# Kernel tuning notes

Measured on AMD Instinct MI355X. Metric: run time of the kernel, lower is better.

Reference implementation:

```python
import jax, jax.numpy as jnp
import numpy as np

N_ITERATIONS = 3
EPS = 1e-07


def squash(t, axis=-1):
    sqr_norm = jnp.sum(t * t, axis=axis, keepdims=True)
    norm = jnp.sqrt(sqr_norm + EPS)
    return sqr_norm * t / ((1.0 + sqr_norm) * norm)


def setup_inputs() -> dict:
    key = jax.random.key(0)
    B, N_IN, N_OUT, D = 256, 1152, 10, 16
    u_hat = jax.random.normal(key, (B, N_IN, N_OUT, D, 1), dtype=jnp.float32)
    return {"u_hat": u_hat}


def reference(u_hat):
    # u_hat: [B, n_in, n_out, d, 1]
    B, n_in, n_out = u_hat.shape[0], u_hat.shape[1], u_hat.shape[2]
    b = jnp.zeros((B, n_in, n_out, 1, 1), dtype=u_hat.dtype)
    v = None
    for r in range(N_ITERATIONS):
        c = jax.nn.softmax(b, axis=1)                      # softmax over input caps
        s = jnp.sum(c * u_hat, axis=1, keepdims=True)      # [B, 1, n_out, d, 1]
        v = squash(s, axis=-2)                             # squash over capsule dim
        if r < N_ITERATIONS - 1:
            # u_hat^T @ v (broadcast v over input caps): agreement [B, n_in, n_out, 1, 1]
            a = jnp.sum(u_hat * v, axis=-2, keepdims=True)
            b = b + a
    return jnp.squeeze(v, axis=1)                          # [B, n_out, d, 1]
```

## Files before the change

kernel.cpp:

```cpp
#include <hip/hip_runtime.h>

#define BATCH 256
#define NIN   1152
#define NOUT  10
#define DDIM  16
#define KPT   18

__global__ __launch_bounds__(256)
void routing_kernel(const float* __restrict__ u_hat, float* __restrict__ out) {
    __shared__ float bsh[NIN];
    __shared__ float wsh[NIN];
    __shared__ float red[4 * DDIM];
    __shared__ float vsh[DDIM];
    __shared__ float scal[8];

    const int t    = threadIdx.x;
    const int q    = t & 3;
    const int g    = t >> 2;
    const int wave = t >> 6;
    const int lane = t & 63;

    const int bb = blockIdx.x / NOUT;
    const int oo = blockIdx.x % NOUT;

    const float* base = u_hat + (size_t)bb * (NIN * NOUT * DDIM) + oo * DDIM + q * 4;

    float4 u[KPT];
#pragma unroll
    for (int k = 0; k < KPT; ++k) {
        const int i = g + 64 * k;
        u[k] = *reinterpret_cast<const float4*>(base + (size_t)i * (NOUT * DDIM));
    }

    for (int i = t; i < NIN; i += 256) bsh[i] = 0.0f;
    __syncthreads();

    for (int r = 0; r < 3; ++r) {
        float m = -3.4e38f;
        for (int i = t; i < NIN; i += 256) m = fmaxf(m, bsh[i]);
        for (int off = 32; off >= 1; off >>= 1) m = fmaxf(m, __shfl_down(m, off));
        if (lane == 0) scal[wave] = m;
        __syncthreads();
        m = fmaxf(fmaxf(scal[0], scal[1]), fmaxf(scal[2], scal[3]));

        float z = 0.0f;
        for (int i = t; i < NIN; i += 256) {
            const float w = __expf(bsh[i] - m);
            wsh[i] = w;
            z += w;
        }
        for (int off = 32; off >= 1; off >>= 1) z += __shfl_down(z, off);
        if (lane == 0) scal[4 + wave] = z;
        __syncthreads();
        const float invZ = 1.0f / (scal[4] + scal[5] + scal[6] + scal[7]);

        float sx = 0.f, sy = 0.f, sz = 0.f, sw = 0.f;
#pragma unroll
        for (int k = 0; k < KPT; ++k) {
            const float w = wsh[g + 64 * k];
            sx += w * u[k].x; sy += w * u[k].y; sz += w * u[k].z; sw += w * u[k].w;
        }
        for (int off = 32; off >= 4; off >>= 1) {
            sx += __shfl_down(sx, off);
            sy += __shfl_down(sy, off);
            sz += __shfl_down(sz, off);
            sw += __shfl_down(sw, off);
        }
        if (lane < 4) {
            float* rp = &red[wave * DDIM + lane * 4];
            rp[0] = sx; rp[1] = sy; rp[2] = sz; rp[3] = sw;
        }
        __syncthreads();
        if (t < DDIM) {
            vsh[t] = (red[t] + red[DDIM + t] + red[2 * DDIM + t] + red[3 * DDIM + t]) * invZ;
        }
        __syncthreads();

        float sqr = 0.0f;
#pragma unroll
        for (int d = 0; d < DDIM; ++d) { const float sv = vsh[d]; sqr += sv * sv; }
        const float scale = sqr / ((1.0f + sqr) * sqrtf(sqr + 1e-7f));
        __syncthreads();
        if (t < DDIM) vsh[t] *= scale;
        __syncthreads();

        if (r == 2) break;

        const float vx = vsh[q * 4 + 0], vy = vsh[q * 4 + 1];
        const float vz = vsh[q * 4 + 2], vw = vsh[q * 4 + 3];
#pragma unroll
        for (int k = 0; k < KPT; ++k) {
            float a = u[k].x * vx + u[k].y * vy + u[k].z * vz + u[k].w * vw;
            a += __shfl_xor(a, 1);
            a += __shfl_xor(a, 2);
            if (q == 0) bsh[g + 64 * k] += a;
        }
        __syncthreads();
    }

    if (t < DDIM) {
        out[(size_t)blockIdx.x * DDIM + t] = vsh[t];
    }
}

extern "C" void kernel_launch(void* const* d_in, const int* in_sizes, int n_in,
                              void* d_out, int out_size, void* d_ws, size_t ws_size,
                              hipStream_t stream) {
    const float* u_hat = (const float*)d_in[0];
    float* out = (float*)d_out;
    routing_kernel<<<dim3(BATCH * NOUT), dim3(256), 0, stream>>>(u_hat, out);
}
```

Measured before the change: 261.2 us.

## Process two output capsules per block for contiguous 128-byte loads

```diff
diff --git a/kernel.cpp b/kernel.cpp
--- a/kernel.cpp
+++ b/kernel.cpp
@@ -1,105 +1,130 @@
 #include <hip/hip_runtime.h>
 
-#define BATCH 256
 #define NIN   1152
 #define NOUT  10
-#define DDIM  16
 #define KPT   18
 
-__global__ __launch_bounds__(256)
+__global__ __launch_bounds__(512, 4)
 void routing_kernel(const float* __restrict__ u_hat, float* __restrict__ out) {
-    __shared__ float bsh[NIN];
-    __shared__ float wsh[NIN];
-    __shared__ float red[4 * DDIM];
-    __shared__ float vsh[DDIM];
-    __shared__ float scal[8];
+    __shared__ float bsh[2][NIN];
+    __shared__ float wsh[2][NIN];
+    __shared__ __align__(16) float red[8][2][16];
+    __shared__ __align__(16) float vsh[2][16];
+    __shared__ float msc[8][2];
+    __shared__ float zsc[8][2];
 
     const int t    = threadIdx.x;
     const int q    = t & 3;
-    const int g    = t >> 2;
+    const int o    = (t >> 2) & 1;
+    const int g    = t >> 3;
     const int wave = t >> 6;
     const int lane = t & 63;
 
-    const int bb = blockIdx.x / NOUT;
-    const int oo = blockIdx.x % NOUT;
+    const int bb = blockIdx.x / 5;
+    const int p  = blockIdx.x % 5;
 
-    const float* base = u_hat + (size_t)bb * (NIN * NOUT * DDIM) + oo * DDIM + q * 4;
+    const float* base = u_hat + (size_t)bb * (NIN * NOUT * 16) + p * 32 + (t & 7) * 4;
 
     float4 u[KPT];
 #pragma unroll
     for (int k = 0; k < KPT; ++k) {
-        const int i = g + 64 * k;
-        u[k] = *reinterpret_cast<const float4*>(base + (size_t)i * (NOUT * DDIM));
+        u[k] = *reinterpret_cast<const float4*>(base + (size_t)(g + 64 * k) * 160);
     }
 
-    for (int i = t; i < NIN; i += 256) bsh[i] = 0.0f;
+    for (int i = t; i < 2 * NIN; i += 512) (&bsh[0][0])[i] = 0.0f;
     __syncthreads();
+
+    const int tid_o = q + (g << 2);
 
     for (int r = 0; r < 3; ++r) {
         float m = -3.4e38f;
-        for (int i = t; i < NIN; i += 256) m = fmaxf(m, bsh[i]);
-        for (int off = 32; off >= 1; off >>= 1) m = fmaxf(m, __shfl_down(m, off));
-        if (lane == 0) scal[wave] = m;
+        for (int i = tid_o; i < NIN; i += 256) m = fmaxf(m, bsh[o][i]);
+        m = fmaxf(m, __shfl_down(m, 32));
+        m = fmaxf(m, __shfl_down(m, 16));
+        m = fmaxf(m, __shfl_down(m, 8));
+        m = fmaxf(m, __shfl_xor(m, 1));
+        m = fmaxf(m, __shfl_xor(m, 2));
+        if (lane == 0 || lane == 4) msc[wave][(lane >> 2) & 1] = m;
         __syncthreads();
-        m = fmaxf(fmaxf(scal[0], scal[1]), fmaxf(scal[2], scal[3]));
+        float M = msc[0][o];
+#pragma unroll
+        for (int w = 1; w < 8; ++w) M = fmaxf(M, msc[w][o]);
 
         float z = 0.0f;
-        for (int i = t; i < NIN; i += 256) {
-            const float w = __expf(bsh[i] - m);
-            wsh[i] = w;
+        for (int i = tid_o; i < NIN; i += 256) {
+            const float w = __expf(bsh[o][i] - M);
+            wsh[o][i] = w;
             z += w;
         }
-        for (int off = 32; off >= 1; off >>= 1) z += __shfl_down(z, off);
-        if (lane == 0) scal[4 + wave] = z;
+        z += __shfl_down(z, 32);
+        z += __shfl_down(z, 16);
+        z += __shfl_down(z, 8);
+        z += __shfl_xor(z, 1);
+        z += __shfl_xor(z, 2);
+        if (lane == 0 || lane == 4) zsc[wave][(lane >> 2) & 1] = z;
         __syncthreads();
-        const float invZ = 1.0f / (scal[4] + scal[5] + scal[6] + scal[7]);
+        float Z = 0.0f;
+#pragma unroll
+        for (int w = 0; w < 8; ++w) Z += zsc[w][o];
+        const float invZ = 1.0f / Z;
 
         float sx = 0.f, sy = 0.f, sz = 0.f, sw = 0.f;
 #pragma unroll
         for (int k = 0; k < KPT; ++k) {
-            const float w = wsh[g + 64 * k];
+            const float w = wsh[o][g + 64 * k];
             sx += w * u[k].x; sy += w * u[k].y; sz += w * u[k].z; sw += w * u[k].w;
         }
-        for (int off = 32; off >= 4; off >>= 1) {
+        for (int off = 32; off >= 8; off >>= 1) {
             sx += __shfl_down(sx, off);
             sy += __shfl_down(sy, off);
             sz += __shfl_down(sz, off);
             sw += __shfl_down(sw, off);
         }
-        if (lane < 4) {
-            float* rp = &red[wave * DDIM + lane * 4];
-            rp[0] = sx; rp[1] = sy; rp[2] = sz; rp[3] = sw;
+        if (lane < 8) {
+            float4 sv; sv.x = sx; sv.y = sy; sv.z = sz; sv.w = sw;
+            *reinterpret_cast<float4*>(&red[wave][(lane >> 2) & 1][(lane & 3) * 4]) = sv;
         }
         __syncthreads();
-        if (t < DDIM) {
-            vsh[t] = (red[t] + red[DDIM + t] + red[2 * DDIM + t] + red[3 * DDIM + t]) * invZ;
+        if (t < 32) {
+            const int oi = t >> 4, d = t & 15;
+            float acc = 0.0f;
+#pragma unroll
+            for (int w = 0; w < 8; ++w) acc += red[w][oi][d];
+            float Zo = 0.0f;
+#pragma unroll
+            for (int w = 0; w < 8; ++w) Zo += zsc[w][oi];
+            vsh[oi][d] = acc / Zo;
         }
         __syncthreads();
 
-        float sqr = 0.0f;
+        float sq0 = 0.f, sq1 = 0.f;
 #pragma unroll
-        for (int d = 0; d < DDIM; ++d) { const float sv = vsh[d]; sqr += sv * sv; }
-        const float scale = sqr / ((1.0f + sqr) * sqrtf(sqr + 1e-7f));
-        __syncthreads();
-        if (t < DDIM) vsh[t] *= scale;
-        __syncthreads();
+        for (int d = 0; d < 16; ++d) {
+            const float a0 = vsh[0][d], a1 = vsh[1][d];
+            sq0 += a0 * a0; sq1 += a1 * a1;
+        }
+        const float sc0 = sq0 / ((1.0f + sq0) * sqrtf(sq0 + 1e-7f));
+        const float sc1 = sq1 / ((1.0f + sq1) * sqrtf(sq1 + 1e-7f));
 
-        if (r == 2) break;
+        if (r == 2) {
+            if (t < 32) {
+                const int oi = t >> 4, d = t & 15;
+                out[((size_t)bb * NOUT + 2 * p + oi) * 16 + d] =
+                    vsh[oi][d] * (oi ? sc1 : sc0);
+            }
+            break;
+        }
 
-        const float vx = vsh[q * 4 + 0], vy = vsh[q * 4 + 1];
-        const float vz = vsh[q * 4 + 2], vw = vsh[q * 4 + 3];
+        const float scale = o ? sc1 : sc0;
+        const float4 vq = *reinterpret_cast<const float4*>(&vsh[o][q * 4]);
 #pragma unroll
         for (int k = 0; k < KPT; ++k) {
-            float a = u[k].x * vx + u[k].y * vy + u[k].z * vz + u[k].w * vw;
+            float a = u[k].x * vq.x + u[k].y * vq.y + u[k].z * vq.z + u[k].w * vq.w;
             a += __shfl_xor(a, 1);
             a += __shfl_xor(a, 2);
-            if (q == 0) bsh[g + 64 * k] += a;
+            if (q == 0) bsh[o][g + 64 * k] += a * scale;
         }
         __syncthreads();
-    }
-
-    if (t < DDIM) {
-        out[(size_t)blockIdx.x * DDIM + t] = vsh[t];
     }
 }
 
@@ -108,5 +133,5 @@
                               hipStream_t stream) {
     const float* u_hat = (const float*)d_in[0];
     float* out = (float*)d_out;
-    routing_kernel<<<dim3(BATCH * NOUT), dim3(256), 0, stream>>>(u_hat, out);
+    routing_kernel<<<dim3(256 * 5), dim3(512), 0, stream>>>(u_hat, out);
 }
```

Result: no change. 262.9 us (+0.6%).

## Split routing into streaming pass and combine kernels using cumulative v

Applied to the files above, without the earlier changes.

```diff
diff --git a/kernel.cpp b/kernel.cpp
--- a/kernel.cpp
+++ b/kernel.cpp
@@ -1,112 +1,132 @@
 #include <hip/hip_runtime.h>
 
-#define BATCH 256
-#define NIN   1152
-#define NOUT  10
-#define DDIM  16
-#define KPT   18
+#define NB   256
+#define NIN  1152
+#define NOUT 10
+#define NCH  12
+#define KST  3
 
+
+template<int MODE>
 __global__ __launch_bounds__(256)
-void routing_kernel(const float* __restrict__ u_hat, float* __restrict__ out) {
-    __shared__ float bsh[NIN];
-    __shared__ float wsh[NIN];
-    __shared__ float red[4 * DDIM];
-    __shared__ float vsh[DDIM];
-    __shared__ float scal[8];
+void pass_kernel(const float* __restrict__ u_hat, const float* __restrict__ V,
+                 float* __restrict__ P) {
+    __shared__ float red[256 * 5 * 5];
 
-    const int t    = threadIdx.x;
-    const int q    = t & 3;
-    const int g    = t >> 2;
-    const int wave = t >> 6;
-    const int lane = t & 63;
+    const int t  = threadIdx.x;
+    const int q  = t & 3;
+    const int p0 = t >> 2;
+    const int bb = blockIdx.x / NCH;
+    const int c  = blockIdx.x % NCH;
 
-    const int bb = blockIdx.x / NOUT;
-    const int oo = blockIdx.x % NOUT;
-
-    const float* base = u_hat + (size_t)bb * (NIN * NOUT * DDIM) + oo * DDIM + q * 4;
-
-    float4 u[KPT];
+    float4 Vq[5];
 #pragma unroll
-    for (int k = 0; k < KPT; ++k) {
-        const int i = g + 64 * k;
-        u[k] = *reinterpret_cast<const float4*>(base + (size_t)i * (NOUT * DDIM));
+    for (int j = 0; j < 5; ++j) {
+        if (MODE) {
+            const int oo = (p0 + 4 * j) % 10;
+            Vq[j] = *reinterpret_cast<const float4*>(V + ((bb * NOUT + oo) * 16) + q * 4);
+        }
     }
 
-    for (int i = t; i < NIN; i += 256) bsh[i] = 0.0f;
+    float  Z[5];
+    float4 S[5];
+#pragma unroll
+    for (int j = 0; j < 5; ++j) { Z[j] = 0.f; S[j] = make_float4(0.f, 0.f, 0.f, 0.f); }
+
+    const float4* up = reinterpret_cast<const float4*>(u_hat);
+    const size_t base = (size_t)bb * 46080 + c * 3840 + t;
+
+    for (int k = 0; k < KST; ++k) {
+#pragma unroll
+        for (int j = 0; j < 5; ++j) {
+            const float4 u4 = up[base + k * 1280 + j * 256];
+            float e;
+            if (MODE) {
+                float d = u4.x * Vq[j].x + u4.y * Vq[j].y + u4.z * Vq[j].z + u4.w * Vq[j].w;
+                d += __shfl_xor(d, 1);
+                d += __shfl_xor(d, 2);
+                e = __expf(d);
+            } else {
+                e = 1.0f;
+            }
+            Z[j]   += e;
+            S[j].x += e * u4.x; S[j].y += e * u4.y;
+            S[j].z += e * u4.z; S[j].w += e * u4.w;
+        }
+    }
+
+#pragma unroll
+    for (int j = 0; j < 5; ++j) {
+        float* r = &red[(t * 5 + j) * 5];
+        r[0] = Z[j]; r[1] = S[j].x; r[2] = S[j].y; r[3] = S[j].z; r[4] = S[j].w;
+    }
     __syncthreads();
 
-    for (int r = 0; r < 3; ++r) {
-        float m = -3.4e38f;
-        for (int i = t; i < NIN; i += 256) m = fmaxf(m, bsh[i]);
-        for (int off = 32; off >= 1; off >>= 1) m = fmaxf(m, __shfl_down(m, off));
-        if (lane == 0) scal[wave] = m;
-        __syncthreads();
-        m = fmaxf(fmaxf(scal[0], scal[1]), fmaxf(scal[2], scal[3]));
+    if (t < 40) {
+        const int oo = t >> 2, qq = t & 3;
+        float acc0 = 0.f, acc1 = 0.f, acc2 = 0.f, acc3 = 0.f, acc4 = 0.f;
+        for (int p = (oo & 1); p < 64; p += 2) {
+            const int dd = (oo - p + 70) % 10;
+            const int j  = ((dd >> 1) * 3) % 5;
+            const float* r = &red[((p * 4 + qq) * 5 + j) * 5];
+            acc0 += r[0]; acc1 += r[1]; acc2 += r[2]; acc3 += r[3]; acc4 += r[4];
+        }
+        float* o = &P[(((size_t)c * NB + bb) * 40 + t) * 5];
+        o[0] = acc0; o[1] = acc1; o[2] = acc2; o[3] = acc3; o[4] = acc4;
+    }
+}
 
-        float z = 0.0f;
-        for (int i = t; i < NIN; i += 256) {
-            const float w = __expf(bsh[i] - m);
-            wsh[i] = w;
-            z += w;
+template<int R>
+__global__ __launch_bounds__(64)
+void combine_kernel(const float* __restrict__ P, const float* __restrict__ Vprev,
+                    float* __restrict__ Vnext, float* __restrict__ out) {
+    const int t  = threadIdx.x;
+    const int bb = blockIdx.x;
+    if (t >= 40) return;
+    const int oo = t >> 2, q = t & 3;
+
+    float Z = 0.f;
+    float4 S = make_float4(0.f, 0.f, 0.f, 0.f);
+    for (int c = 0; c < NCH; ++c) {
+        const float* r = &P[(((size_t)c * NB + bb) * 40 + t) * 5];
+        Z += r[0]; S.x += r[1]; S.y += r[2]; S.z += r[3]; S.w += r[4];
+    }
+    const float inv = 1.0f / Z;
+    const float4 s = make_float4(S.x * inv, S.y * inv, S.z * inv, S.w * inv);
+
+    float pr = s.x * s.x + s.y * s.y + s.z * s.z + s.w * s.w;
+    pr += __shfl_xor(pr, 1);
+    pr += __shfl_xor(pr, 2);
+    const float scale = pr / ((1.0f + pr) * sqrtf(pr + 1e-7f));
+    float4 v = make_float4(s.x * scale, s.y * scale, s.z * scale, s.w * scale);
+
+    if (R == 2) {
+        *reinterpret_cast<float4*>(out + ((size_t)bb * NOUT + oo) * 16 + q * 4) = v;
+    } else {
+        if (R == 1) {
+            const float4 Vp = *reinterpret_cast<const float4*>(
+                Vprev + ((bb * NOUT + oo) * 16) + q * 4);
+            v.x += Vp.x; v.y += Vp.y; v.z += Vp.z; v.w += Vp.w;
         }
-        for (int off = 32; off >= 1; off >>= 1) z += __shfl_down(z, off);
-        if (lane == 0) scal[4 + wave] = z;
-        __syncthreads();
-        const float invZ = 1.0f / (scal[4] + scal[5] + scal[6] + scal[7]);
-
-        float sx = 0.f, sy = 0.f, sz = 0.f, sw = 0.f;
-#pragma unroll
-        for (int k = 0; k < KPT; ++k) {
-            const float w = wsh[g + 64 * k];
-            sx += w * u[k].x; sy += w * u[k].y; sz += w * u[k].z; sw += w * u[k].w;
-        }
-        for (int off = 32; off >= 4; off >>= 1) {
-            sx += __shfl_down(sx, off);
-            sy += __shfl_down(sy, off);
-            sz += __shfl_down(sz, off);
-            sw += __shfl_down(sw, off);
-        }
-        if (lane < 4) {
-            float* rp = &red[wave * DDIM + lane * 4];
-            rp[0] = sx; rp[1] = sy; rp[2] = sz; rp[3] = sw;
-        }
-        __syncthreads();
-        if (t < DDIM) {
-            vsh[t] = (red[t] + red[DDIM + t] + red[2 * DDIM + t] + red[3 * DDIM + t]) * invZ;
-        }
-        __syncthreads();
-
-        float sqr = 0.0f;
-#pragma unroll
-        for (int d = 0; d < DDIM; ++d) { const float sv = vsh[d]; sqr += sv * sv; }
-        const float scale = sqr / ((1.0f + sqr) * sqrtf(sqr + 1e-7f));
-        __syncthreads();
-        if (t < DDIM) vsh[t] *= scale;
-        __syncthreads();
-
-        if (r == 2) break;
-
-        const float vx = vsh[q * 4 + 0], vy = vsh[q * 4 + 1];
-        const float vz = vsh[q * 4 + 2], vw = vsh[q * 4 + 3];
-#pragma unroll
-        for (int k = 0; k < KPT; ++k) {
-            float a = u[k].x * vx + u[k].y * vy + u[k].z * vz + u[k].w * vw;
-            a += __shfl_xor(a, 1);
-            a += __shfl_xor(a, 2);
-            if (q == 0) bsh[g + 64 * k] += a;
-        }
-        __syncthreads();
-    }
-
-    if (t < DDIM) {
-        out[(size_t)blockIdx.x * DDIM + t] = vsh[t];
+        *reinterpret_cast<float4*>(Vnext + ((bb * NOUT + oo) * 16) + q * 4) = v;
     }
 }
 
 extern "C" void kernel_launch(void* const* d_in, const int* in_sizes, int n_in,
                               void* d_out, int out_size, void* d_ws, size_t ws_size,
                               hipStream_t stream) {
-    const float* u_hat = (const float*)d_in[0];
+    const float* u = (const float*)d_in[0];
     float* out = (float*)d_out;
-    routing_kernel<<<dim3(BATCH * NOUT), dim3(256), 0, stream>>>(u_hat, out);
+    float* ws  = (float*)d_ws;
+    float* V1  = ws;
+    float* V2  = ws + 40960;
+    float* P   = ws + 81920;
+
+    const dim3 pg(NB * NCH), pb(256), cg(NB), cb(64);
+    pass_kernel<0><<<pg, pb, 0, stream>>>(u, nullptr, P);
+    combine_kernel<0><<<cg, cb, 0, stream>>>(P, nullptr, V1, nullptr);
+    pass_kernel<1><<<pg, pb, 0, stream>>>(u, V1, P);
+    combine_kernel<1><<<cg, cb, 0, stream>>>(P, V1, V2, nullptr);
+    pass_kernel<1><<<pg, pb, 0, stream>>>(u, V2, P);
+    combine_kernel<2><<<cg, cb, 0, stream>>>(P, nullptr, nullptr, out);
 }
```

Result: slower. 322.2 us (+23.3%).
